# Performance work log

Hardware: AMD Instinct MI355X
Metric: run time of the kernel (lower is better)

The kernel has to match this reference:

```python
import jax, jax.numpy as jnp
import numpy as np

N_NODES = 10000
N_EDGES = 320000
FIN = 2
HID = 64
OUT = 16
B = 4
T = 12


def _gcn_norm(src, dst, w, n):
    # add self loops (fill value 1.0, improved=False), then symmetric normalization
    loop = jnp.arange(n, dtype=src.dtype)
    src = jnp.concatenate([src, loop])
    dst = jnp.concatenate([dst, loop])
    w = jnp.concatenate([w, jnp.ones((n,), w.dtype)])
    deg = jax.ops.segment_sum(w, dst, num_segments=n)
    dinv = jnp.where(deg > 0, 1.0 / jnp.sqrt(deg), 0.0)
    return src, dst, dinv[src] * w * dinv[dst]


def _gcn_conv(x_nbf, src, dst, norm, W, b, n):
    # x_nbf: [N,B,F] ; GCNConv: (x W) aggregated with normalized weights, + bias
    xw = jnp.einsum('nbf,fh->nbh', x_nbf, W)          # [N,B,H]
    msgs = xw[src] * norm[:, None, None]               # [E',B,H]
    return jax.ops.segment_sum(msgs, dst, num_segments=n) + b


def setup_inputs() -> dict:
    key = jax.random.key(0)
    ks = jax.random.split(key, 20)
    x = jax.random.normal(ks[0], (B, N_NODES, FIN, T), jnp.float32)
    edge_index = jax.random.randint(ks[1], (2, N_EDGES), 0, N_NODES, jnp.int64 if jax.config.jax_enable_x64 else jnp.int32)
    edge_weight = jax.random.uniform(ks[2], (N_EDGES,), jnp.float32)
    s = 0.1
    p = {
        'Wz': s * jax.random.normal(ks[3], (FIN, HID), jnp.float32),
        'bz': jnp.zeros((HID,), jnp.float32),
        'Wr': s * jax.random.normal(ks[4], (FIN, HID), jnp.float32),
        'br': jnp.zeros((HID,), jnp.float32),
        'Wh': s * jax.random.normal(ks[5], (FIN, HID), jnp.float32),
        'bh': jnp.zeros((HID,), jnp.float32),
        'Lz_w': s * jax.random.normal(ks[6], (2 * HID, HID), jnp.float32),
        'Lz_b': jnp.zeros((HID,), jnp.float32),
        'Lr_w': s * jax.random.normal(ks[7], (2 * HID, HID), jnp.float32),
        'Lr_b': jnp.zeros((HID,), jnp.float32),
        'Lh_w': s * jax.random.normal(ks[8], (2 * HID, HID), jnp.float32),
        'Lh_b': jnp.zeros((HID,), jnp.float32),
        'lin_w': s * jax.random.normal(ks[9], (HID, OUT), jnp.float32),
        'lin_b': jnp.zeros((OUT,), jnp.float32),
    }
    return dict(x=x, edge_index=edge_index, edge_weight=edge_weight, **p)


def reference(x, edge_index, edge_weight, Wz, bz, Wr, br, Wh, bh,
              Lz_w, Lz_b, Lr_w, Lr_b, Lh_w, Lh_b, lin_w, lin_b):
    Bd, N, Fin, Td = x.shape
    src, dst, norm = _gcn_norm(edge_index[0], edge_index[1], edge_weight, N)
    H0 = jnp.zeros((N, Bd, Wz.shape[1]), x.dtype)
    xs = jnp.transpose(x, (3, 1, 0, 2))  # [T,N,B,Fin]

    def step(H, xt):
        cz = _gcn_conv(xt, src, dst, norm, Wz, bz, N)
        Z = jax.nn.sigmoid(jnp.concatenate([cz, H], -1) @ Lz_w + Lz_b)
        cr = _gcn_conv(xt, src, dst, norm, Wr, br, N)
        R = jax.nn.sigmoid(jnp.concatenate([cr, H], -1) @ Lr_w + Lr_b)
        ch = _gcn_conv(xt, src, dst, norm, Wh, bh, N)
        H_tilde = jnp.tanh(jnp.concatenate([ch, H * R], -1) @ Lh_w + Lh_b)
        Hn = Z * H + (1.0 - Z) * H_tilde
        out_t = jax.nn.relu(Hn) @ lin_w + lin_b  # [N,B,OUT]
        return Hn, out_t

    _, outs = jax.lax.scan(step, H0, xs)        # [T,N,B,OUT]
    return jnp.transpose(outs, (2, 0, 1, 3))     # [B,T,N,OUT]
```

## Files before the change

kernel.cpp:

```cpp
#include <hip/hip_runtime.h>
#include <cstdint>
#include <cstddef>

#define NN      10000
#define NE      320000
#define FINF    2
#define HIDN    64
#define OUTN    16
#define BBATCH  4
#define TSTEPS  12
#define NBROWS  (NN * BBATCH)
#define XTN     (TSTEPS * NN * BBATCH * FINF)
#define CAP     96

typedef _Float16 v8h __attribute__((ext_vector_type(8)));
typedef _Float16 v2h __attribute__((ext_vector_type(2)));
typedef float    v4f __attribute__((ext_vector_type(4)));

extern "C" __global__ void setup_kernel(const float* __restrict__ x,
                             const int* __restrict__ src, const int* __restrict__ dst,
                             const float* __restrict__ ew,
                             int* __restrict__ cnt, float* __restrict__ degf,
                             int2* __restrict__ bucket, _Float16* __restrict__ xAll,
                             const float* __restrict__ Wz, const float* __restrict__ bz,
                             const float* __restrict__ Wr, const float* __restrict__ br,
                             const float* __restrict__ Wh, const float* __restrict__ bh,
                             const float* __restrict__ Lz, const float* __restrict__ Lz_b,
                             const float* __restrict__ Lr, const float* __restrict__ Lr_b,
                             const float* __restrict__ Lh, const float* __restrict__ Lh_b,
                             const float* __restrict__ linw, const float* __restrict__ linb,
                             float* __restrict__ PP) {
    int idx = blockIdx.x * 256 + threadIdx.x;
    if (idx < BBATCH * NN) {
        int b = idx / NN;
        int n = idx - b * NN;
        const float* xp = x + (size_t)idx * (FINF * TSTEPS);
        v2h* xo = (v2h*)xAll;
        #pragma unroll
        for (int t = 0; t < TSTEPS; ++t) {
            v2h p;
            p.x = (_Float16)xp[t];
            p.y = (_Float16)xp[TSTEPS + t];
            xo[n * 48 + t * 4 + b] = p;
        }
    }
    if (idx < NE) {
        int d = dst[idx];
        int s = src[idx];
        float w = ew[idx];
        int p = atomicAdd(&cnt[d], 1);
        if (p < CAP) {
            int2 rec;
            rec.x = s;
            rec.y = __float_as_int(w);
            bucket[d * CAP + p] = rec;
        }
        atomicAdd(&degf[d], w);
    }
    if (idx < 13904) {
        const float* Lg[3]    = {Lz, Lr, Lh};
        const float* Lbias[3] = {Lz_b, Lr_b, Lh_b};
        const float* Wg[3]    = {Wz, Wr, Wh};
        const float* bg[3]    = {bz, br, bh};
        int i = idx;
        if (i < 12288) {
            int g = i >> 12, rr = (i >> 6) & 63, j = i & 63;
            PP[i] = Lg[g][(64 + rr) * 64 + j];
        } else if (i < 12672) {
            int i2 = i - 12288;
            int g = i2 >> 7, f = (i2 >> 6) & 1, j = i2 & 63;
            float s = 0.f;
            for (int k = 0; k < 64; ++k) s = fmaf(Wg[g][f * 64 + k], Lg[g][k * 64 + j], s);
            PP[i] = s;
        } else if (i < 12864) {
            int i3 = i - 12672;
            int g = i3 >> 6, j = i3 & 63;
            float s = Lbias[g][j];
            for (int k = 0; k < 64; ++k) s = fmaf(bg[g][k], Lg[g][k * 64 + j], s);
            PP[i] = s;
        } else if (i < 13888) {
            PP[i] = linw[i - 12864];
        } else {
            PP[i] = linb[i - 13888];
        }
    }
}

__device__ __forceinline__ float fsigmoid(float x) {
    return 1.0f / (1.0f + __expf(-x));
}

extern "C" __global__ __launch_bounds__(256, 3)
void fused_kernel(const _Float16* __restrict__ xAll, const int2* __restrict__ bucket,
                  const int* __restrict__ cnt, const float* __restrict__ degf,
                  const float* __restrict__ PP, float* __restrict__ out) {
    __shared__ _Float16 WTH[64 * 72 + 32];
    __shared__ _Float16 WIZR[2 * 64 * 8 + 32];
    __shared__ _Float16 Hm[4][16 * 72];
    __shared__ float    aggL[16 * 96];
    __shared__ int      s_src[16 * CAP];
    __shared__ float    s_c[16 * CAP];
    __shared__ int      s_cnt[16];
    const int tid = threadIdx.x;
    const int w   = tid >> 6;
    const int l   = tid & 63;
    const int m   = l & 15;
    const int q   = l >> 4;
    const int n0  = blockIdx.x * 16 + w * 4 + q;

    {
        const int nl = tid >> 4;
        const int u  = tid & 15;
        const int ng = blockIdx.x * 16 + nl;
        const int c  = min(cnt[ng], CAP);
        if (u == 0) s_cnt[nl] = c;
        const float dn = rsqrtf(1.0f + degf[ng]);
        for (int i = u; i < c; i += 16) {
            int2 rec = bucket[ng * CAP + i];
            int s = rec.x;
            s_src[nl * CAP + i] = s;
            s_c[nl * CAP + i]   = __int_as_float(rec.y) * dn * rsqrtf(1.0f + degf[s]);
        }
    }

    for (int i = tid; i < 4096; i += 256) {
        int k = i >> 6, n = i & 63;
        WTH[n * 72 + k] = (_Float16)PP[8192 + i];
    }
    for (int i = tid; i < 64 * 8; i += 256) {
        int n = i >> 3, kk = i & 7;
        float v = 0.f;
        if (kk == 0)      v = PP[12288 + 2 * 128 + n];
        else if (kk == 1) v = PP[12288 + 2 * 128 + 64 + n];
        else if (kk == 2) v = PP[12672 + 2 * 64 + n];
        WTH[n * 72 + 64 + kk] = (_Float16)v;
    }
    for (int i = tid; i < 32; i += 256) WTH[64 * 72 + i] = (_Float16)0.f;
    for (int i = tid; i < 2 * 64 * 8; i += 256) {
        int g = i >> 9, rem = i & 511, n = rem >> 3, kk = rem & 7;
        float v = 0.f;
        if (kk == 0)      v = PP[12288 + g * 128 + n];
        else if (kk == 1) v = PP[12288 + g * 128 + 64 + n];
        else if (kk == 2) v = PP[12672 + g * 64 + n];
        WIZR[(g * 64 + n) * 8 + kk] = (_Float16)v;
    }
    for (int i = tid; i < 32; i += 256) WIZR[1024 + i] = (_Float16)0.f;

    __syncthreads();

    {
        const int nl = tid >> 4;
        const int u  = tid & 15;
        const int ng = blockIdx.x * 16 + nl;
        const int c  = s_cnt[nl];
        const float dn = rsqrtf(1.0f + degf[ng]);
        const v2h* x2 = (const v2h*)xAll;
        float acc[6];
        {
            v2h a = x2[(size_t)ng * 48 + u * 3];
            v2h b = x2[(size_t)ng * 48 + u * 3 + 1];
            v2h e = x2[(size_t)ng * 48 + u * 3 + 2];
            float c0 = dn * dn;
            acc[0] = c0 * (float)a.x; acc[1] = c0 * (float)a.y;
            acc[2] = c0 * (float)b.x; acc[3] = c0 * (float)b.y;
            acc[4] = c0 * (float)e.x; acc[5] = c0 * (float)e.y;
        }
        for (int i = 0; i < c; ++i) {
            int s    = s_src[nl * CAP + i];
            float cc = s_c[nl * CAP + i];
            v2h a = x2[(size_t)s * 48 + u * 3];
            v2h b = x2[(size_t)s * 48 + u * 3 + 1];
            v2h e = x2[(size_t)s * 48 + u * 3 + 2];
            acc[0] = fmaf(cc, (float)a.x, acc[0]);
            acc[1] = fmaf(cc, (float)a.y, acc[1]);
            acc[2] = fmaf(cc, (float)b.x, acc[2]);
            acc[3] = fmaf(cc, (float)b.y, acc[3]);
            acc[4] = fmaf(cc, (float)e.x, acc[4]);
            acc[5] = fmaf(cc, (float)e.y, acc[5]);
        }
        #pragma unroll
        for (int jj = 0; jj < 6; ++jj) aggL[nl * 96 + u * 6 + jj] = acc[jj];
    }

    v8h BZ[4][2], BR[4][2];
    #pragma unroll
    for (int nt = 0; nt < 4; ++nt) {
        #pragma unroll
        for (int c = 0; c < 2; ++c) {
            #pragma unroll
            for (int i = 0; i < 8; ++i) {
                int k = c * 32 + q * 8 + i;
                BZ[nt][c][i] = (_Float16)PP[k * 64 + nt * 16 + m];
                BR[nt][c][i] = (_Float16)PP[4096 + k * 64 + nt * 16 + m];
            }
        }
    }
    v8h linB0, linB1;
    #pragma unroll
    for (int i = 0; i < 8; ++i) {
        linB0[i] = (_Float16)PP[12864 + (q * 8 + i) * 16 + m];
        linB1[i] = (_Float16)PP[12864 + (32 + q * 8 + i) * 16 + m];
    }
    const float linbv = PP[13888 + m];

    __syncthreads();

    _Float16* __restrict__ Hw = &Hm[w][0];
    const int wsw = (q & 2) << 3;
    const _Float16* __restrict__ Ard = Hw + m * 72 + ((q ^ ((m >> 2) & 2)) * 8);
    const int aggBase = (w * 4 + (m >> 2)) * 96 + (m & 3) * 2;

    float Hold[4][4];
    #pragma unroll
    for (int nt = 0; nt < 4; ++nt)
        #pragma unroll
        for (int r = 0; r < 4; ++r) Hold[nt][r] = 0.f;
    v8h aH0{}, aH1{};

    const v4f zeroc = {0.f, 0.f, 0.f, 0.f};

    for (int t = 0; t < TSTEPS; ++t) {
        v8h aI{};
        if (q == 0) {
            const float2 av = *(const float2*)&aggL[aggBase + t * 8];
            aI[0] = (_Float16)av.x;
            aI[1] = (_Float16)av.y;
            aI[2] = (_Float16)1.0f;
        }

        v4f accZ[4], accR[4];
        #pragma unroll
        for (int nt = 0; nt < 4; ++nt) {
            const v8h bIz = *(const v8h*)&WIZR[(0 * 64 + nt * 16 + m) * 8 + q * 8];
            const v8h bIr = *(const v8h*)&WIZR[(1 * 64 + nt * 16 + m) * 8 + q * 8];
            accZ[nt] = __builtin_amdgcn_mfma_f32_16x16x32_f16(aI,  bIz,       zeroc,    0, 0, 0);
            accZ[nt] = __builtin_amdgcn_mfma_f32_16x16x32_f16(aH0, BZ[nt][0], accZ[nt], 0, 0, 0);
            accZ[nt] = __builtin_amdgcn_mfma_f32_16x16x32_f16(aH1, BZ[nt][1], accZ[nt], 0, 0, 0);
            accR[nt] = __builtin_amdgcn_mfma_f32_16x16x32_f16(aI,  bIr,       zeroc,    0, 0, 0);
            accR[nt] = __builtin_amdgcn_mfma_f32_16x16x32_f16(aH0, BR[nt][0], accR[nt], 0, 0, 0);
            accR[nt] = __builtin_amdgcn_mfma_f32_16x16x32_f16(aH1, BR[nt][1], accR[nt], 0, 0, 0);
        }

        float Z[4][4];
        #pragma unroll
        for (int nt = 0; nt < 4; ++nt) {
            #pragma unroll
            for (int r = 0; r < 4; ++r) {
                Z[nt][r] = fsigmoid(accZ[nt][r]);
                float hr = Hold[nt][r] * fsigmoid(accR[nt][r]);
                Hw[(q * 4 + r) * 72 + ((nt * 16 + m) ^ wsw)] = (_Float16)hr;
            }
        }
        __threadfence_block();
        const v8h aP0 = *(const v8h*)Ard;
        const v8h aP1 = *(const v8h*)(Ard + 32);

        v4f accH[4];
        #pragma unroll
        for (int nt = 0; nt < 4; ++nt) {
            const _Float16* bh = &WTH[(nt * 16 + m) * 72 + q * 8];
            accH[nt] = __builtin_amdgcn_mfma_f32_16x16x32_f16(aI,  *(const v8h*)(bh + 64), zeroc,    0, 0, 0);
            accH[nt] = __builtin_amdgcn_mfma_f32_16x16x32_f16(aP0, *(const v8h*)bh,        accH[nt], 0, 0, 0);
            accH[nt] = __builtin_amdgcn_mfma_f32_16x16x32_f16(aP1, *(const v8h*)(bh + 32), accH[nt], 0, 0, 0);
        }

        #pragma unroll
        for (int nt = 0; nt < 4; ++nt) {
            #pragma unroll
            for (int r = 0; r < 4; ++r) {
                float ht = fmaf(2.0f, fsigmoid(2.0f * accH[nt][r]), -1.0f);
                float hn = Z[nt][r] * Hold[nt][r] + (1.f - Z[nt][r]) * ht;
                Hold[nt][r] = hn;
                Hw[(q * 4 + r) * 72 + ((nt * 16 + m) ^ wsw)] = (_Float16)hn;
            }
        }
        __threadfence_block();
        aH0 = *(const v8h*)Ard;
        aH1 = *(const v8h*)(Ard + 32);

        const v8h zz{};
        v8h r0 = __builtin_elementwise_max(aH0, zz);
        v8h r1 = __builtin_elementwise_max(aH1, zz);
        v4f accO = {linbv, linbv, linbv, linbv};
        accO = __builtin_amdgcn_mfma_f32_16x16x32_f16(r0, linB0, accO, 0, 0, 0);
        accO = __builtin_amdgcn_mfma_f32_16x16x32_f16(r1, linB1, accO, 0, 0, 0);
        #pragma unroll
        for (int r = 0; r < 4; ++r)
            out[(((size_t)r * TSTEPS + t) * NN + n0) * 16 + m] = accO[r];
    }
}


extern "C" void kernel_launch(void* const* d_in, const int* in_sizes, int n_in,
                              void* d_out, int out_size, void* d_ws, size_t ws_size,
                              hipStream_t stream) {
    const float* x   = (const float*)d_in[0];
    const int*   ei  = (const int*)d_in[1];
    const float* ew  = (const float*)d_in[2];
    const float* Wz  = (const float*)d_in[3];
    const float* bz  = (const float*)d_in[4];
    const float* Wr  = (const float*)d_in[5];
    const float* br  = (const float*)d_in[6];
    const float* Wh  = (const float*)d_in[7];
    const float* bh  = (const float*)d_in[8];
    const float* Lz  = (const float*)d_in[9];
    const float* Lz_b= (const float*)d_in[10];
    const float* Lr  = (const float*)d_in[11];
    const float* Lr_b= (const float*)d_in[12];
    const float* Lh  = (const float*)d_in[13];
    const float* Lh_b= (const float*)d_in[14];
    const float* lw  = (const float*)d_in[15];
    const float* lb  = (const float*)d_in[16];
    float* out = (float*)d_out;

    char* ws = (char*)d_ws;
    size_t off = 0;
    auto alloc = [&](size_t bytes) -> char* {
        char* p = ws + off;
        off += (bytes + 15) & ~(size_t)15;
        return p;
    };
    _Float16* xAll = (_Float16*)alloc((size_t)XTN * 2);
    float* PP      = (float*)alloc(13904 * 4);
    int2*  bucket  = (int2*) alloc((size_t)NN * CAP * 8);
    int*   cnt     = (int*)  alloc(NN * 4);
    float* degf    = (float*)alloc(NN * 4);

    const int* srcp = ei;
    const int* dstp = ei + NE;

    hipMemsetAsync(cnt, 0, 2 * NN * sizeof(int), stream);
    setup_kernel<<<(NE + 255) / 256, 256, 0, stream>>>(x, srcp, dstp, ew, cnt, degf,
                                                       bucket, xAll,
                                                       Wz, bz, Wr, br, Wh, bh,
                                                       Lz, Lz_b, Lr, Lr_b, Lh, Lh_b,
                                                       lw, lb, PP);
    fused_kernel<<<NN / 16, 256, 0, stream>>>(xAll, bucket, cnt, degf, PP, out);
}
```

Measured before the change: 221.2 us.

## Vectorize x transpose, use raw exp2/rcp sigmoid, strength-reduce output indexing

The setup transpose now uses one thread per node. Each thread loads each batch's 24 floats as vector loads and writes 12 contiguous 16-byte fp16 vectors, replacing scattered 4-byte stores. The sigmoid uses the hardware exp2 and reciprocal builtins instead of __expf and a division, which drops the IEEE-accurate divide. Output addressing uses an incrementing pointer instead of recomputing the full index each step. The raw rcp/exp2 may change precision slightly, and the transpose now runs on fewer threads.

```diff
diff --git a/kernel.cpp b/kernel.cpp
--- a/kernel.cpp
+++ b/kernel.cpp
@@ -31,18 +31,27 @@
                              const float* __restrict__ linw, const float* __restrict__ linb,
                              float* __restrict__ PP) {
     int idx = blockIdx.x * 256 + threadIdx.x;
-    if (idx < BBATCH * NN) {
-        int b = idx / NN;
-        int n = idx - b * NN;
-        const float* xp = x + (size_t)idx * (FINF * TSTEPS);
-        v2h* xo = (v2h*)xAll;
-        #pragma unroll
-        for (int t = 0; t < TSTEPS; ++t) {
-            v2h p;
-            p.x = (_Float16)xp[t];
-            p.y = (_Float16)xp[TSTEPS + t];
-            xo[n * 48 + t * 4 + b] = p;
-        }
+    if (idx < NN) {
+        const int n = idx;
+        v8h* xo = (v8h*)(xAll + (size_t)n * 96);
+        v8h vv[TSTEPS];
+        #pragma unroll
+        for (int b = 0; b < BBATCH; ++b) {
+            const v4f* xp4 = (const v4f*)(x + ((size_t)b * NN + n) * 24);
+            v4f c0 = xp4[0], c1 = xp4[1], c2 = xp4[2];
+            v4f c3 = xp4[3], c4 = xp4[4], c5 = xp4[5];
+            float f0[TSTEPS] = {c0.x, c0.y, c0.z, c0.w, c1.x, c1.y, c1.z, c1.w,
+                                c2.x, c2.y, c2.z, c2.w};
+            float f1[TSTEPS] = {c3.x, c3.y, c3.z, c3.w, c4.x, c4.y, c4.z, c4.w,
+                                c5.x, c5.y, c5.z, c5.w};
+            #pragma unroll
+            for (int t = 0; t < TSTEPS; ++t) {
+                vv[t][b * 2]     = (_Float16)f0[t];
+                vv[t][b * 2 + 1] = (_Float16)f1[t];
+            }
+        }
+        #pragma unroll
+        for (int t = 0; t < TSTEPS; ++t) xo[t] = vv[t];
     }
     if (idx < NE) {
         int d = dst[idx];
@@ -87,7 +96,7 @@
 }
 
 __device__ __forceinline__ float fsigmoid(float x) {
-    return 1.0f / (1.0f + __expf(-x));
+    return __builtin_amdgcn_rcpf(1.0f + __builtin_amdgcn_exp2f(-1.442695041f * x));
 }
 
 extern "C" __global__ __launch_bounds__(256, 3)
@@ -218,6 +227,7 @@
     v8h aH0{}, aH1{};
 
     const v4f zeroc = {0.f, 0.f, 0.f, 0.f};
+    float* __restrict__ op = out + (size_t)n0 * 16 + m;
 
     for (int t = 0; t < TSTEPS; ++t) {
         v8h aI{};
@@ -286,7 +296,8 @@
         accO = __builtin_amdgcn_mfma_f32_16x16x32_f16(r1, linB1, accO, 0, 0, 0);
         #pragma unroll
         for (int r = 0; r < 4; ++r)
-            out[(((size_t)r * TSTEPS + t) * NN + n0) * 16 + m] = accO[r];
+            op[(size_t)r * (TSTEPS * NN * 16)] = accO[r];
+        op += NN * 16;
     }
 }
 
```

Result: faster. 193.8 us (-12.4%).
